# Performance work log

Hardware: AMD Instinct MI355X
Metric: run time of the kernel (lower is better)

The kernel has to match this reference:

```python
import jax, jax.numpy as jnp
import numpy as np
from jax import lax

CIN, COUT, K_EXP, KSZ = 128, 256, 8, 3
HIDDEN = CIN // 4  # reduction=4
B, H, W = 32, 56, 56
TEMP = 1.0


def setup_inputs() -> dict:
    key = jax.random.key(0)
    ks = jax.random.split(key, 6)
    x = jax.random.normal(ks[0], (B, CIN, H, W), dtype=jnp.float32)
    weight_bank = jax.random.normal(ks[1], (K_EXP, COUT, CIN, KSZ, KSZ), dtype=jnp.float32) * 0.02
    fc1_w = jax.random.normal(ks[2], (HIDDEN, CIN), dtype=jnp.float32) * (1.0 / np.sqrt(CIN))
    fc1_b = jnp.zeros((HIDDEN,), dtype=jnp.float32)
    fc2_w = jax.random.normal(ks[3], (K_EXP, HIDDEN), dtype=jnp.float32) * (1.0 / np.sqrt(HIDDEN))
    fc2_b = jnp.zeros((K_EXP,), dtype=jnp.float32)
    return {"x": x, "weight_bank": weight_bank, "fc1_w": fc1_w, "fc1_b": fc1_b,
            "fc2_w": fc2_w, "fc2_b": fc2_b}


def reference(x, weight_bank, fc1_w, fc1_b, fc2_w, fc2_b):
    b, cin, h, w = x.shape
    # Routing: GAP -> fc1 -> relu -> fc2 -> softmax(/T)
    v = jnp.mean(x, axis=(2, 3))                       # (B, cin)
    hdd = jax.nn.relu(v @ fc1_w.T + fc1_b)             # (B, hidden)
    logits = hdd @ fc2_w.T + fc2_b                     # (B, K)
    a = jax.nn.softmax(logits / TEMP, axis=1)          # (B, K)
    # Per-sample dynamic weights: (B, cout, cin, k, k)
    Wdyn = jnp.einsum('bk,kocij->bocij', a, weight_bank)
    # Batched per-sample conv via grouped convolution:
    # x -> (1, B*cin, H, W), Wdyn -> (B*cout, cin, k, k), groups=B
    xg = x.reshape(1, b * cin, h, w)
    wg = Wdyn.reshape(b * weight_bank.shape[1], cin, KSZ, KSZ)
    y = lax.conv_general_dilated(
        xg, wg,
        window_strides=(1, 1),
        padding=[(1, 1), (1, 1)],
        feature_group_count=b,
        dimension_numbers=('NCHW', 'OIHW', 'NCHW'),
    )
    return y.reshape(b, weight_bank.shape[1], y.shape[2], y.shape[3])
```

## Files before the change

### kernel.cpp

```cpp
#include <hip/hip_runtime.h>


#define CIN    128
#define COUT   256
#define KEXP   8
#define HIDDEN 32
#define B_     32
#define H_     56
#define W_     56
#define HW     3136
#define HP     58
#define WP     58
#define KK     1152

typedef float  v4f  __attribute__((ext_vector_type(4)));
typedef __bf16 v8bf __attribute__((ext_vector_type(8)));

__device__ __forceinline__ unsigned short f2bf(float x) {
  unsigned int u = __float_as_uint(x);
  u += 0x7fff + ((u >> 16) & 1);
  return (unsigned short)(u >> 16);
}

__device__ __forceinline__ void gl_lds16(const void* g, void* lds) {
  __builtin_amdgcn_global_load_lds(
      (__attribute__((address_space(1))) void*)(unsigned long long)(g),
      (__attribute__((address_space(3))) void*)(lds),
      16, 0, 0);
}

__global__ __launch_bounds__(256) void k_xpose(const float* __restrict__ x,
                                               unsigned short* __restrict__ xpt,
                                               float* __restrict__ gpart) {
  const int h = blockIdx.x, b = blockIdx.y, tid = threadIdx.x;
  __shared__ float tf[56 * 129];
  __shared__ float gp[256];
  const float4* xr4 = (const float4*)x + (size_t)b * CIN * 784;

#pragma unroll
  for (int it = 0; it < 7; ++it) {
    int idx = it * 256 + tid;
    int c  = idx / 14;
    int wq = idx - c * 14;
    float4 q = xr4[(size_t)c * 784 + h * 14 + wq];
    int w0 = wq * 4;
    tf[(w0 + 0) * 129 + c] = q.x;
    tf[(w0 + 1) * 129 + c] = q.y;
    tf[(w0 + 2) * 129 + c] = q.z;
    tf[(w0 + 3) * 129 + c] = q.w;
  }
  __syncthreads();

  {
    int c = tid & 127, half = tid >> 7;
    float s = 0.f;
#pragma unroll
    for (int w = half * 28; w < half * 28 + 28; ++w) s += tf[w * 129 + c];
    gp[tid] = s;
  }

#pragma unroll
  for (int it = 0; it < 7; ++it) {
    int idx = it * 256 + tid;
    int w  = idx >> 5;
    int c4 = (idx & 31) << 2;
    ushort4 o;
    o.x = f2bf(tf[w * 129 + c4 + 0]);
    o.y = f2bf(tf[w * 129 + c4 + 1]);
    o.z = f2bf(tf[w * 129 + c4 + 2]);
    o.w = f2bf(tf[w * 129 + c4 + 3]);
    *(ushort4*)(xpt + ((size_t)(b * HP + (h + 1)) * WP + (w + 1)) * CIN + c4) = o;
  }

  if (tid < 128) {
    size_t rb = (size_t)(b * HP + (h + 1)) * WP * CIN;
    xpt[rb + tid] = 0;
    xpt[rb + 57 * CIN + tid] = 0;
  }
  if (h == 0 || h == 55) {
    int hr = (h == 0) ? 0 : 57;
    size_t rb = (size_t)(b * HP + hr) * WP * CIN;
    ushort4 z; z.x = z.y = z.z = z.w = 0;
    for (int i = tid; i < 1856; i += 256)
      *(ushort4*)(xpt + rb + i * 4) = z;
  }

  __syncthreads();
  if (tid < 128)
    gpart[((size_t)h * B_ + b) * CIN + tid] =
        (gp[tid] + gp[tid + 128]) * (1.0f / 3136.0f);
}

__global__ void k_mlp(const float* __restrict__ gpart, const float* __restrict__ fc1w,
                      const float* __restrict__ fc1b, const float* __restrict__ fc2w,
                      const float* __restrict__ fc2b, float* __restrict__ aout) {
  const int b = blockIdx.x, t = threadIdx.x;
  __shared__ float vS[CIN];
  __shared__ float hid[HIDDEN];
  __shared__ float lg[KEXP];
  {
    float s = 0.f;
    for (int h = 0; h < H_; ++h) s += gpart[((size_t)h * B_ + b) * CIN + t];
    vS[t] = s;
  }
  __syncthreads();
  if (t < HIDDEN) {
    float s = fc1b[t];
    const float* wr = fc1w + t * CIN;
    for (int c = 0; c < CIN; ++c) s += vS[c] * wr[c];
    hid[t] = fmaxf(s, 0.f);
  }
  __syncthreads();
  if (t < KEXP) {
    float s = fc2b[t];
    const float* wr = fc2w + t * HIDDEN;
    for (int j = 0; j < HIDDEN; ++j) s += hid[j] * wr[j];
    lg[t] = s;
  }
  __syncthreads();
  if (t == 0) {
    float m = lg[0];
    for (int k = 1; k < KEXP; ++k) m = fmaxf(m, lg[k]);
    float e[KEXP], den = 0.f;
    for (int k = 0; k < KEXP; ++k) { e[k] = expf(lg[k] - m); den += e[k]; }
    float inv = 1.0f / den;
    for (int k = 0; k < KEXP; ++k) aout[b * KEXP + k] = e[k] * inv;
  }
}

__global__ __launch_bounds__(512) void k_wdyn(const float* __restrict__ aout,
                                              const float* __restrict__ bank,
                                              unsigned short* __restrict__ wdyn) {
  const int cout = blockIdx.x, tid = threadIdx.x;
  __shared__ float4 bS4[KEXP * 288];
  __shared__ float aS[B_ * KEXP];

  for (int idx = tid; idx < KEXP * 288; idx += 512) {
    int k = idx / 288, r = idx - k * 288;
    bS4[idx] = ((const float4*)(bank + (size_t)(k * COUT + cout) * KK))[r];
  }
  if (tid < 256) aS[tid] = aout[tid];
  __syncthreads();

  const float* bS = (const float*)bS4;
  const int lane_kk = tid & 63;
  const int sg = tid >> 6;
  float areg[4][KEXP];
#pragma unroll
  for (int bi = 0; bi < 4; ++bi)
#pragma unroll
    for (int k = 0; k < KEXP; ++k) areg[bi][k] = aS[(sg * 4 + bi) * KEXP + k];

  for (int it = 0; it < 18; ++it) {
    int kk  = it * 64 + lane_kk;
    int khw = kk >> 7, cin = kk & 127;
    int e   = cin * 9 + khw;
    float vv[KEXP];
#pragma unroll
    for (int k = 0; k < KEXP; ++k) vv[k] = bS[k * KK + e];
#pragma unroll
    for (int bi = 0; bi < 4; ++bi) {
      float s = 0.f;
#pragma unroll
      for (int k = 0; k < KEXP; ++k) s += areg[bi][k] * vv[k];
      wdyn[(size_t)((sg * 4 + bi) * COUT + cout) * KK + kk] = f2bf(s);
    }
  }
}

#define BARX()   asm volatile("s_barrier" ::: "memory")
#define WAITV2() asm volatile("s_waitcnt vmcnt(2)" ::: "memory")
#define WAITV0() asm volatile("s_waitcnt vmcnt(0)" ::: "memory")

__device__ __forceinline__ void stage_a(const unsigned short* wb, unsigned short* Abuf,
                                        int hf, int ad, const int (&aoffj)[2], int wv) {
  const unsigned short* s = wb + hf * 128 * KK + ad;
  unsigned short* d = Abuf + hf * 8192;
  gl_lds16(s + aoffj[0], d + (wv * 64) * 8);
  gl_lds16(s + aoffj[1], d + (512 + wv * 64) * 8);
}

__device__ __forceinline__ void stage_b(const unsigned short* xb, unsigned short* Bbuf,
                                        int hf, int bd, const int (&boffj)[2][2], int wv) {
  unsigned short* d = Bbuf + hf * 8192;
  gl_lds16(xb + boffj[0][hf] + bd, d + (wv * 64) * 8);
  gl_lds16(xb + boffj[1][hf] + bd, d + (512 + wv * 64) * 8);
}

template <int MH>
__device__ __forceinline__ void load_a(const unsigned short* Ab, int abase, int pA, int pB,
                                       v8bf (&af)[4][2]) {
#pragma unroll
  for (int mi = 0; mi < 4; ++mi) {
    int r = abase + (MH * 4 + mi) * 1024;
    af[mi][0] = *(const v8bf*)(Ab + r + pA);
    af[mi][1] = *(const v8bf*)(Ab + r + pB);
  }
}

template <int NH>
__device__ __forceinline__ void load_b(const unsigned short* Bb, int bbase, int pA, int pB,
                                       v8bf (&bv)[2][2]) {
#pragma unroll
  for (int ni = 0; ni < 2; ++ni) {
    int r = bbase + (NH * 2 + ni) * 1024;
    bv[ni][0] = *(const v8bf*)(Bb + r + pA);
    bv[ni][1] = *(const v8bf*)(Bb + r + pB);
  }
}

template <int MH, int NH>
__device__ __forceinline__ void mfma_q(v8bf (&af)[4][2], v8bf (&bv)[2][2],
                                       v4f (&acc)[8][4]) {
  __builtin_amdgcn_s_setprio(1);
#pragma unroll
  for (int mi = 0; mi < 4; ++mi)
#pragma unroll
    for (int ni = 0; ni < 2; ++ni) {
      v4f& a = acc[MH * 4 + mi][NH * 2 + ni];
      a = __builtin_amdgcn_mfma_f32_16x16x32_bf16(af[mi][0], bv[ni][0], a, 0, 0, 0);
      a = __builtin_amdgcn_mfma_f32_16x16x32_bf16(af[mi][1], bv[ni][1], a, 0, 0, 0);
    }
  __builtin_amdgcn_s_setprio(0);
}

__global__ __launch_bounds__(512, 2) void k_conv256(const unsigned short* __restrict__ wdyn,
                                                    const unsigned short* __restrict__ xpt,
                                                    float* __restrict__ out) {
  extern __shared__ unsigned short sh[];
  unsigned short* As = sh;
  unsigned short* Bs = sh + 32768;

  const int id  = blockIdx.x;
  const int xcd = id & 7, idx = id >> 3;
  const int b   = xcd * 4 + idx / 13;
  const int ch  = idx - (idx / 13) * 13;
  const int p0  = ch << 8;

  const int tid = threadIdx.x;
  const int wv = tid >> 6, l = tid & 63;
  const int q4 = l >> 4, l15 = l & 15;
  const int wr = wv >> 2, wc = wv & 3;

  const unsigned short* wb = wdyn + (size_t)b * COUT * KK;
  const unsigned short* xb = xpt + (size_t)b * HP * WP * CIN;

  int aoffj[2];
  int boffj[2][2];
#pragma unroll
  for (int j = 0; j < 2; ++j) {
    int row0 = j * 64 + (tid >> 3);
    int c = (tid & 7) ^ (row0 & 7);
    aoffj[j] = row0 * KK + c * 8;
#pragma unroll
    for (int hf = 0; hf < 2; ++hf) {
      int p = p0 + hf * 128 + row0;
      p = p > 3135 ? 3135 : p;
      int ph = p / 56, pw = p - ph * 56;
      boffj[j][hf] = (ph * WP + pw) * CIN + c * 8;
    }
  }

  const int abase = (wr * 128 + l15) * 64;
  const int bbase = (wc * 64 + l15) * 64;
  const int s7 = l15 & 7;
  const int pA = (q4 ^ s7) * 8;
  const int pB = ((q4 + 4) ^ s7) * 8;

  v4f acc[8][4];
#pragma unroll
  for (int m = 0; m < 8; ++m)
#pragma unroll
    for (int n = 0; n < 4; ++n)
#pragma unroll
      for (int rr = 0; rr < 4; ++rr) acc[m][n][rr] = 0.f;

  unsigned short* A0 = As;           unsigned short* B0 = Bs;
  unsigned short* A1 = As + 16384;   unsigned short* B1 = Bs + 16384;

  stage_a(wb, A0, 0, 0, aoffj, wv);
  stage_a(wb, A0, 1, 0, aoffj, wv);
  stage_b(xb, B0, 0, 0, boffj, wv);
  stage_b(xb, B0, 1, 0, boffj, wv);
  WAITV0();
  BARX();

  v8bf afA[4][2], bv0[2][2], bv1[2][2];

  auto halftile = [&](const unsigned short* Ab, const unsigned short* Bb,
                      unsigned short* An, unsigned short* Bn,
                      int adS, int bdS, bool doStage) {
    if (doStage) { stage_a(wb, An, 0, adS, aoffj, wv); WAITV2(); }
    else         { WAITV0(); }
    BARX();
    load_a<0>(Ab, abase, pA, pB, afA);
    load_b<0>(Bb, bbase, pA, pB, bv0);
    mfma_q<0, 0>(afA, bv0, acc);
    BARX();
    load_b<1>(Bb, bbase, pA, pB, bv1);
    if (doStage) stage_a(wb, An, 1, adS, aoffj, wv);
    BARX();
    mfma_q<0, 1>(afA, bv1, acc);
    BARX();
    load_a<1>(Ab, abase, pA, pB, afA);
    if (doStage) stage_b(xb, Bn, 0, bdS, boffj, wv);
    BARX();
    mfma_q<1, 1>(afA, bv1, acc);
    BARX();
    if (doStage) stage_b(xb, Bn, 1, bdS, boffj, wv);
    BARX();
    mfma_q<1, 0>(afA, bv0, acc);
    BARX();
  };

  int kh = 0, kw = 0;
  for (int i = 0; i < 9; ++i) {
    int kw2 = kw + 1, kh2 = kh;
    if (kw2 == 3) { kw2 = 0; kh2 = kh + 1; }
    const int adO = (2 * i + 1) * 64;
    const int adN = (2 * i + 2) * 64;
    const int bdO = (kh * WP + kw) * CIN + 64;
    const int bdN = (kh2 * WP + kw2) * CIN;

    halftile(A0, B0, A1, B1, adO, bdO, true);
    halftile(A1, B1, A0, B0, adN, bdN, i != 8);

    kh = kh2; kw = kw2;
  }

#pragma unroll
  for (int mf = 0; mf < 8; ++mf) {
    int cout = wr * 128 + mf * 16 + 4 * q4;
#pragma unroll
    for (int nf = 0; nf < 4; ++nf) {
      int p = p0 + wc * 64 + nf * 16 + l15;
      if (p < HW) {
        float* op = out + (size_t)(b * COUT + cout) * HW + p;
#pragma unroll
        for (int rr = 0; rr < 4; ++rr) op[(size_t)rr * HW] = acc[mf][nf][rr];
      }
    }
  }
}

extern "C" void kernel_launch(void* const* d_in, const int* in_sizes, int n_in,
                              void* d_out, int out_size, void* d_ws, size_t ws_size,
                              hipStream_t stream) {
  const float* x    = (const float*)d_in[0];
  const float* bank = (const float*)d_in[1];
  const float* fc1w = (const float*)d_in[2];
  const float* fc1b = (const float*)d_in[3];
  const float* fc2w = (const float*)d_in[4];
  const float* fc2b = (const float*)d_in[5];
  float* out = (float*)d_out;

  char* ws = (char*)d_ws;
  float* gpart = (float*)(ws + 0);
  float* aout  = (float*)(ws + (1u << 20));
  unsigned short* wdyn = (unsigned short*)(ws + (2u << 20));
  unsigned short* xpt  = (unsigned short*)(ws + (2u << 20) + 18874368);

  static bool attr_done = false;
  if (!attr_done) {
    (void)hipFuncSetAttribute((const void*)k_conv256,
                              hipFuncAttributeMaxDynamicSharedMemorySize, 131072);
    attr_done = true;
  }

  k_xpose<<<dim3(H_, B_), 256, 0, stream>>>(x, xpt, gpart);
  k_mlp<<<dim3(B_), 128, 0, stream>>>(gpart, fc1w, fc1b, fc2w, fc2b, aout);
  k_wdyn<<<dim3(COUT), 512, 0, stream>>>(aout, bank, wdyn);
  k_conv256<<<dim3(416), 512, 131072, stream>>>(wdyn, xpt, out);
}
```

Before: 228.8 us.

## Shrink conv GEMM tile to 128x128 with 256 threads and fewer barriers

Replaces the 256x256 output tile per block (512 threads, 416 blocks) with a 128x128 tile (256 threads, 1600 blocks), splitting cout into two halves and pixels into 128-wide chunks. Staging is consolidated into one helper that issues four loads per operand per k-step, and most intra-tile barriers are removed. The aim is better load balance across CUs, less wave-quantization tail, and less barrier overhead. In exchange, each tile reuses less data from LDS, so global and L2 traffic per FLOP roughly doubles, and the 128-wide pixel chunks add padding waste at the tail (25*128 vs 3136).

```diff
diff --git a/kernel.cpp b/kernel.cpp
--- a/kernel.cpp
+++ b/kernel.cpp
@@ -169,30 +169,22 @@
 }
 
 #define BARX()   asm volatile("s_barrier" ::: "memory")
-#define WAITV2() asm volatile("s_waitcnt vmcnt(2)" ::: "memory")
+#define WAITV4() asm volatile("s_waitcnt vmcnt(4)" ::: "memory")
 #define WAITV0() asm volatile("s_waitcnt vmcnt(0)" ::: "memory")
 
-__device__ __forceinline__ void stage_a(const unsigned short* wb, unsigned short* Abuf,
-                                        int hf, int ad, const int (&aoffj)[2], int wv) {
-  const unsigned short* s = wb + hf * 128 * KK + ad;
-  unsigned short* d = Abuf + hf * 8192;
-  gl_lds16(s + aoffj[0], d + (wv * 64) * 8);
-  gl_lds16(s + aoffj[1], d + (512 + wv * 64) * 8);
-}
-
-__device__ __forceinline__ void stage_b(const unsigned short* xb, unsigned short* Bbuf,
-                                        int hf, int bd, const int (&boffj)[2][2], int wv) {
-  unsigned short* d = Bbuf + hf * 8192;
-  gl_lds16(xb + boffj[0][hf] + bd, d + (wv * 64) * 8);
-  gl_lds16(xb + boffj[1][hf] + bd, d + (512 + wv * 64) * 8);
+__device__ __forceinline__ void stage4(const unsigned short* src, unsigned short* dbuf,
+                                       const int (&off)[4], int disp, int tid) {
+#pragma unroll
+  for (int g = 0; g < 4; ++g)
+    gl_lds16(src + off[g] + disp, dbuf + (g * 256 + tid) * 8);
 }
 
 template <int MH>
 __device__ __forceinline__ void load_a(const unsigned short* Ab, int abase, int pA, int pB,
-                                       v8bf (&af)[4][2]) {
-#pragma unroll
-  for (int mi = 0; mi < 4; ++mi) {
-    int r = abase + (MH * 4 + mi) * 1024;
+                                       v8bf (&af)[2][2]) {
+#pragma unroll
+  for (int mi = 0; mi < 2; ++mi) {
+    int r = abase + (MH * 2 + mi) * 1024;
     af[mi][0] = *(const v8bf*)(Ab + r + pA);
     af[mi][1] = *(const v8bf*)(Ab + r + pB);
   }
@@ -210,105 +202,95 @@
 }
 
 template <int MH, int NH>
-__device__ __forceinline__ void mfma_q(v8bf (&af)[4][2], v8bf (&bv)[2][2],
-                                       v4f (&acc)[8][4]) {
+__device__ __forceinline__ void mfma_q(v8bf (&af)[2][2], v8bf (&bv)[2][2],
+                                       v4f (&acc)[4][4]) {
   __builtin_amdgcn_s_setprio(1);
 #pragma unroll
-  for (int mi = 0; mi < 4; ++mi)
+  for (int mi = 0; mi < 2; ++mi)
 #pragma unroll
     for (int ni = 0; ni < 2; ++ni) {
-      v4f& a = acc[MH * 4 + mi][NH * 2 + ni];
+      v4f& a = acc[MH * 2 + mi][NH * 2 + ni];
       a = __builtin_amdgcn_mfma_f32_16x16x32_bf16(af[mi][0], bv[ni][0], a, 0, 0, 0);
       a = __builtin_amdgcn_mfma_f32_16x16x32_bf16(af[mi][1], bv[ni][1], a, 0, 0, 0);
     }
   __builtin_amdgcn_s_setprio(0);
 }
 
-__global__ __launch_bounds__(512, 2) void k_conv256(const unsigned short* __restrict__ wdyn,
+__global__ __launch_bounds__(256, 2) void k_conv128(const unsigned short* __restrict__ wdyn,
                                                     const unsigned short* __restrict__ xpt,
                                                     float* __restrict__ out) {
   extern __shared__ unsigned short sh[];
   unsigned short* As = sh;
-  unsigned short* Bs = sh + 32768;
+  unsigned short* Bs = sh + 16384;
 
   const int id  = blockIdx.x;
   const int xcd = id & 7, idx = id >> 3;
-  const int b   = xcd * 4 + idx / 13;
-  const int ch  = idx - (idx / 13) * 13;
-  const int p0  = ch << 8;
+  const int bs  = idx / 50;
+  const int r   = idx - bs * 50;
+  const int b   = xcd * 4 + bs;
+  const int bm  = r / 25;
+  const int ch  = r - bm * 25;
+  const int p0  = ch << 7;
 
   const int tid = threadIdx.x;
   const int wv = tid >> 6, l = tid & 63;
   const int q4 = l >> 4, l15 = l & 15;
-  const int wr = wv >> 2, wc = wv & 3;
-
-  const unsigned short* wb = wdyn + (size_t)b * COUT * KK;
+  const int wr = wv >> 1, wc = wv & 1;
+
+  const unsigned short* wb = wdyn + ((size_t)b * COUT + bm * 128) * KK;
   const unsigned short* xb = xpt + (size_t)b * HP * WP * CIN;
 
-  int aoffj[2];
-  int boffj[2][2];
-#pragma unroll
-  for (int j = 0; j < 2; ++j) {
-    int row0 = j * 64 + (tid >> 3);
-    int c = (tid & 7) ^ (row0 & 7);
-    aoffj[j] = row0 * KK + c * 8;
-#pragma unroll
-    for (int hf = 0; hf < 2; ++hf) {
-      int p = p0 + hf * 128 + row0;
-      p = p > 3135 ? 3135 : p;
-      int ph = p / 56, pw = p - ph * 56;
-      boffj[j][hf] = (ph * WP + pw) * CIN + c * 8;
-    }
-  }
-
-  const int abase = (wr * 128 + l15) * 64;
+  int aoff[4], boff[4];
+#pragma unroll
+  for (int g = 0; g < 4; ++g) {
+    int gidx = g * 256 + tid;
+    int row = gidx >> 3;
+    int c = (gidx & 7) ^ (row & 7);
+    aoff[g] = row * KK + c * 8;
+    int p = p0 + row;
+    p = p > 3135 ? 3135 : p;
+    int ph = p / 56, pw = p - ph * 56;
+    boff[g] = (ph * WP + pw) * CIN + c * 8;
+  }
+
+  const int abase = (wr * 64 + l15) * 64;
   const int bbase = (wc * 64 + l15) * 64;
   const int s7 = l15 & 7;
   const int pA = (q4 ^ s7) * 8;
   const int pB = ((q4 + 4) ^ s7) * 8;
 
-  v4f acc[8][4];
-#pragma unroll
-  for (int m = 0; m < 8; ++m)
+  v4f acc[4][4];
+#pragma unroll
+  for (int m = 0; m < 4; ++m)
 #pragma unroll
     for (int n = 0; n < 4; ++n)
 #pragma unroll
       for (int rr = 0; rr < 4; ++rr) acc[m][n][rr] = 0.f;
 
-  unsigned short* A0 = As;           unsigned short* B0 = Bs;
-  unsigned short* A1 = As + 16384;   unsigned short* B1 = Bs + 16384;
-
-  stage_a(wb, A0, 0, 0, aoffj, wv);
-  stage_a(wb, A0, 1, 0, aoffj, wv);
-  stage_b(xb, B0, 0, 0, boffj, wv);
-  stage_b(xb, B0, 1, 0, boffj, wv);
+  unsigned short* A0 = As;          unsigned short* B0 = Bs;
+  unsigned short* A1 = As + 8192;   unsigned short* B1 = Bs + 8192;
+
+  stage4(wb, A0, aoff, 0, tid);
+  stage4(xb, B0, boff, 0, tid);
   WAITV0();
   BARX();
 
-  v8bf afA[4][2], bv0[2][2], bv1[2][2];
-
-  auto halftile = [&](const unsigned short* Ab, const unsigned short* Bb,
-                      unsigned short* An, unsigned short* Bn,
-                      int adS, int bdS, bool doStage) {
-    if (doStage) { stage_a(wb, An, 0, adS, aoffj, wv); WAITV2(); }
+  v8bf afA[2][2], bv0[2][2], bv1[2][2];
+
+  auto tile = [&](const unsigned short* Ab, const unsigned short* Bb,
+                  unsigned short* An, unsigned short* Bn,
+                  int adS, int bdS, bool doStage) {
+    if (doStage) { stage4(wb, An, aoff, adS, tid); WAITV4(); }
     else         { WAITV0(); }
     BARX();
     load_a<0>(Ab, abase, pA, pB, afA);
     load_b<0>(Bb, bbase, pA, pB, bv0);
     mfma_q<0, 0>(afA, bv0, acc);
-    BARX();
     load_b<1>(Bb, bbase, pA, pB, bv1);
-    if (doStage) stage_a(wb, An, 1, adS, aoffj, wv);
-    BARX();
+    if (doStage) stage4(xb, Bn, boff, bdS, tid);
     mfma_q<0, 1>(afA, bv1, acc);
-    BARX();
     load_a<1>(Ab, abase, pA, pB, afA);
-    if (doStage) stage_b(xb, Bn, 0, bdS, boffj, wv);
-    BARX();
     mfma_q<1, 1>(afA, bv1, acc);
-    BARX();
-    if (doStage) stage_b(xb, Bn, 1, bdS, boffj, wv);
-    BARX();
     mfma_q<1, 0>(afA, bv0, acc);
     BARX();
   };
@@ -322,15 +304,15 @@
     const int bdO = (kh * WP + kw) * CIN + 64;
     const int bdN = (kh2 * WP + kw2) * CIN;
 
-    halftile(A0, B0, A1, B1, adO, bdO, true);
-    halftile(A1, B1, A0, B0, adN, bdN, i != 8);
+    tile(A0, B0, A1, B1, adO, bdO, true);
+    tile(A1, B1, A0, B0, adN, bdN, i != 8);
 
     kh = kh2; kw = kw2;
   }
 
 #pragma unroll
-  for (int mf = 0; mf < 8; ++mf) {
-    int cout = wr * 128 + mf * 16 + 4 * q4;
+  for (int mf = 0; mf < 4; ++mf) {
+    int cout = bm * 128 + wr * 64 + mf * 16 + 4 * q4;
 #pragma unroll
     for (int nf = 0; nf < 4; ++nf) {
       int p = p0 + wc * 64 + nf * 16 + l15;
@@ -362,13 +344,13 @@
 
   static bool attr_done = false;
   if (!attr_done) {
-    (void)hipFuncSetAttribute((const void*)k_conv256,
-                              hipFuncAttributeMaxDynamicSharedMemorySize, 131072);
+    (void)hipFuncSetAttribute((const void*)k_conv128,
+                              hipFuncAttributeMaxDynamicSharedMemorySize, 65536);
     attr_done = true;
   }
 
   k_xpose<<<dim3(H_, B_), 256, 0, stream>>>(x, xpt, gpart);
   k_mlp<<<dim3(B_), 128, 0, stream>>>(gpart, fc1w, fc1b, fc2w, fc2b, aout);
   k_wdyn<<<dim3(COUT), 512, 0, stream>>>(aout, bank, wdyn);
-  k_conv256<<<dim3(416), 512, 131072, stream>>>(wdyn, xpt, out);
-}
+  k_conv128<<<dim3(1600), 256, 65536, stream>>>(wdyn, xpt, out);
+}
```

New measurement: 223.4 us. 1.02x faster.
